# Optimization experiments

Measured on AMD Instinct MI355X. Metric: run time of the kernel, lower is better.

Reference implementation:

```python
import jax, jax.numpy as jnp
import numpy as np

# --- configuration constants (match init_kwargs) ---
N = 256          # num_oscillators
T = 200          # simulation steps
INTERVAL = 5     # readout_update_interval
OFFSET = 1       # spike_update_offset
DELAY = 10
D = DELAY + 1    # delay-buffer length
K_GLOBAL = 1.0   # global_coupling_strength
STEP_SIZE = 0.1
GAMMA_ATTR = 0.5 # gamma_attraction_strength
DECAY = 0.9      # membrane_decay
THRESH = 1.0
REC_SCALE = 0.1
ALPHA_FIX = 0.5  # fixed_alpha_value (fixed during training)
CLS_START = 50   # classifier_start_step
SURR_BETA = 4.0  # surrogate-gradient sharpness
NUM_CLASSES = 10


def _spike(u):
    # Heaviside forward, sigmoid surrogate backward (straight-through)
    sg = jax.nn.sigmoid(SURR_BETA * u)
    hard = (u > 0).astype(u.dtype)
    return sg + jax.lax.stop_gradient(hard - sg)


def _forward(x, theta0, W_init, omega, W_ro, W_gate, W_rec, W_fb, W_cls, b_cls):
    B = x.shape[0]
    P = W_gate.shape[1]  # num_pixels = H*W*C
    xf = x.reshape(B, -1)
    gamma0 = jnp.tanh(xf @ W_init)                 # ReadoutLayer.initialize_gamma_from_input -> [B,N]
    buf0 = jnp.tile(theta0[None], (D, 1, 1))       # theta delay buffer [D,B,N]
    zN = jnp.zeros((B, N), x.dtype)
    zP = jnp.zeros((B, P), x.dtype)
    carry0 = (theta0, gamma0, zN, zP, zP, zN, buf0)  # theta, gamma, gate, membrane, spikes, fb-activity a, buffer

    def step(carry, s):
        theta, gamma, gate, mem, spk, a, buf = carry
        # --- KuramotoLayer: dtheta_i = omega_i + K/N * sum_j (1 + W_ij*alpha) sin(th_j - th_i) + attr*gamma_i
        # top-down connectivity W_ij = a_i a_j is rank-1, so the coupling sum is computed exactly in O(N).
        sin_t = jnp.sin(theta); cos_t = jnp.cos(theta)
        S = sin_t.sum(-1, keepdims=True); C = cos_t.sum(-1, keepdims=True)
        base = cos_t * S - sin_t * C
        as_ = jnp.sum(a * sin_t, -1, keepdims=True)
        ac_ = jnp.sum(a * cos_t, -1, keepdims=True)
        weighted = ALPHA_FIX * (cos_t * a * as_ - sin_t * a * ac_)
        dtheta = omega + (K_GLOBAL / N) * (base + weighted) + GAMMA_ATTR * gamma
        theta = theta + STEP_SIZE * dtheta

        # --- ReadoutLayer.gamma_update + SinusoidalGate every INTERVAL steps
        def ro_upd(args):
            g = jnp.tanh(theta @ W_ro)
            gt = g * 0.5 * (1.0 + jnp.cos(theta - buf[0]))  # gate from delayed phase difference
            return g, gt
        gamma, gate = jax.lax.cond((s % INTERVAL) == 0, ro_upd, lambda args: args, (gamma, gate))

        # --- SNNLayer.forward_step + TopDownFeedback on offset spike-update steps
        def sp_upd(args):
            mem_, spk_, a_ = args
            cur = gate @ W_gate + REC_SCALE * (spk_ @ W_rec)
            mem_ = DECAY * mem_ * (1.0 - spk_) + cur       # leaky membrane with reset
            spk_ = _spike(mem_ - THRESH)
            a_ = jnp.tanh(spk_ @ W_fb)                     # per-oscillator feedback activity
            return mem_, spk_, a_
        m_sp = (((s - OFFSET) % INTERVAL) == 0) & (s > OFFSET)
        mem, spk, a = jax.lax.cond(m_sp, sp_upd, lambda args: args, (mem, spk, a))

        buf = jnp.concatenate([buf[1:], theta[None]], axis=0)
        return (theta, gamma, gate, mem, spk, a, buf), spk

    _, spk_hist = jax.lax.scan(step, carry0, jnp.arange(1, T + 1))
    spike_trace = jnp.transpose(spk_hist, (1, 0, 2))       # [B,T,P]
    rate = jnp.mean(spike_trace[:, CLS_START:, :], axis=1) # SNNLayer.classify: mean firing rate
    logits = rate @ W_cls + b_cls
    return logits


def setup_inputs() -> dict:
    key = jax.random.key(0)
    ks = jax.random.split(key, 10)
    B, H, W, C = 32, 32, 32, 3
    P = H * W * C
    x = jax.random.normal(ks[0], (B, H, W, C), jnp.float32)
    theta0 = jax.random.normal(ks[1], (B, N), jnp.float32)
    W_init = jax.random.normal(ks[2], (P, N), jnp.float32) / np.sqrt(P).astype(np.float32)
    omega = jax.random.normal(ks[3], (N,), jnp.float32) * 0.5
    W_ro = jax.random.normal(ks[4], (N, N), jnp.float32) / np.sqrt(N).astype(np.float32)
    W_gate = jax.random.normal(ks[5], (N, P), jnp.float32) / np.sqrt(N).astype(np.float32)
    W_rec = jax.random.normal(ks[6], (P, P), jnp.float32) / np.sqrt(P).astype(np.float32)
    W_fb = jax.random.normal(ks[7], (P, N), jnp.float32) / np.sqrt(P).astype(np.float32)
    W_cls = jax.random.normal(ks[8], (P, NUM_CLASSES), jnp.float32) / np.sqrt(P).astype(np.float32)
    b_cls = jnp.zeros((NUM_CLASSES,), jnp.float32)
    return dict(x=x, theta0=theta0, W_init=W_init, omega=omega, W_ro=W_ro,
                W_gate=W_gate, W_rec=W_rec, W_fb=W_fb, W_cls=W_cls, b_cls=b_cls)


def reference(x, theta0, W_init, omega, W_ro, W_gate, W_rec, W_fb, W_cls, b_cls):
    return _forward(x, theta0, W_init, omega, W_ro, W_gate, W_rec, W_fb, W_cls, b_cls)
```

## Files before the change

### kernel.cpp

```cpp
#include <hip/hip_runtime.h>
#include <cstdint>
#include <cstddef>

#define BB 32
#define NN 256
#define PP 3072
#define NG 192
#define RING 16

typedef unsigned short u16;

__global__ __launch_bounds__(512) void k_init(
    const float* __restrict__ x, const float* __restrict__ W_init,
    double* __restrict__ gpartI, double* __restrict__ memD,
    double* __restrict__ a_g, float* __restrict__ rate,
    u16* __restrict__ maskA, u16* __restrict__ maskB) {
  const int blk = blockIdx.x, tid = threadIdx.x;
  if (blk < 192) {
    const int b = blk / 6, sub = blk % 6;
    __shared__ double xl[512];
    xl[tid] = (double)x[(size_t)b * PP + sub * 512 + tid];
    __syncthreads();
    const int osc = tid & 255, kh = tid >> 8;
    const float* wp = W_init + (size_t)(sub * 512 + kh * 256) * NN + osc;
    const double* xp = xl + kh * 256;
    double a0 = 0, a1 = 0, a2 = 0, a3 = 0, a4 = 0, a5 = 0, a6 = 0, a7 = 0;
    for (int r = 0; r < 256; r += 8) {
      a0 += xp[r + 0] * (double)wp[(size_t)(r + 0) * NN];
      a1 += xp[r + 1] * (double)wp[(size_t)(r + 1) * NN];
      a2 += xp[r + 2] * (double)wp[(size_t)(r + 2) * NN];
      a3 += xp[r + 3] * (double)wp[(size_t)(r + 3) * NN];
      a4 += xp[r + 4] * (double)wp[(size_t)(r + 4) * NN];
      a5 += xp[r + 5] * (double)wp[(size_t)(r + 5) * NN];
      a6 += xp[r + 6] * (double)wp[(size_t)(r + 6) * NN];
      a7 += xp[r + 7] * (double)wp[(size_t)(r + 7) * NN];
    }
    double acc = ((a0 + a1) + (a2 + a3)) + ((a4 + a5) + (a6 + a7));
    __syncthreads();
    __shared__ double hl[256];
    if (kh) hl[osc] = acc;
    __syncthreads();
    if (!kh) gpartI[((size_t)b * 6 + sub) * 256 + osc] = acc + hl[osc];
  } else {
    const int b = blk - 192;
    for (int i = tid; i < PP; i += 512) {
      memD[(size_t)b * PP + i] = 0.0;
      rate[(size_t)b * PP + i] = 0.f;
    }
    for (int i = tid; i < NG; i += 512) {
      maskA[b * NG + i] = 0;
      maskB[b * NG + i] = 0;
    }
    for (int i = tid; i < NN; i += 512) a_g[b * NN + i] = 0.0;
  }
}

__global__ __launch_bounds__(512, 6) void k_rec(
    const float* __restrict__ W_rec, const u16* __restrict__ listG,
    const int* __restrict__ cntG, const int* __restrict__ cntB,
    double* __restrict__ recPart, const double* __restrict__ gateG,
    const float* __restrict__ W_gate, double* __restrict__ gatePart) {
  __shared__ double gd[16 * 130];
  __shared__ float wt[128 * 16];
  __shared__ double red[256];
  const int g = blockIdx.x, bh = blockIdx.y, z = blockIdx.z, j0 = g * 16;
  const int tid = threadIdx.x;

  if (z < 3) {
    const int qd = tid & 3;
    const int h = (tid >> 2) & 7;
    const int bl = tid >> 5;
    const int b = bh * 16 + bl;
    const int beg = (z == 0) ? 0 : cntB[b * 2 + (z - 1)];
    const int end = (z == 2) ? cntG[b] : cntB[b * 2 + z];
    const u16* lst = listG + (size_t)b * PP;
    const float* wp = W_rec + j0 + 4 * qd;

    double a0 = 0, a1 = 0, a2 = 0, a3 = 0;
    int i = beg + h;
    for (; i + 32 <= end; i += 32) {
      const int r0 = lst[i], r1 = lst[i + 8], r2 = lst[i + 16],
                r3 = lst[i + 24];
      const float4 f0 = *(const float4*)(wp + (size_t)r0 * PP);
      const float4 f1 = *(const float4*)(wp + (size_t)r1 * PP);
      const float4 f2 = *(const float4*)(wp + (size_t)r2 * PP);
      const float4 f3 = *(const float4*)(wp + (size_t)r3 * PP);
      a0 += (double)f0.x; a1 += (double)f0.y;
      a2 += (double)f0.z; a3 += (double)f0.w;
      a0 += (double)f1.x; a1 += (double)f1.y;
      a2 += (double)f1.z; a3 += (double)f1.w;
      a0 += (double)f2.x; a1 += (double)f2.y;
      a2 += (double)f2.z; a3 += (double)f2.w;
      a0 += (double)f3.x; a1 += (double)f3.y;
      a2 += (double)f3.z; a3 += (double)f3.w;
    }
    for (; i < end; i += 8) {
      const float4 f = *(const float4*)(wp + (size_t)lst[i] * PP);
      a0 += (double)f.x; a1 += (double)f.y;
      a2 += (double)f.z; a3 += (double)f.w;
    }
    a0 += __shfl_xor(a0, 4); a0 += __shfl_xor(a0, 8); a0 += __shfl_xor(a0, 16);
    a1 += __shfl_xor(a1, 4); a1 += __shfl_xor(a1, 8); a1 += __shfl_xor(a1, 16);
    a2 += __shfl_xor(a2, 4); a2 += __shfl_xor(a2, 8); a2 += __shfl_xor(a2, 16);
    a3 += __shfl_xor(a3, 4); a3 += __shfl_xor(a3, 8); a3 += __shfl_xor(a3, 16);
    if (h == 0) {
      double* dst = recPart + ((size_t)z * BB + b) * PP + j0 + 4 * qd;
      dst[0] = a0; dst[1] = a1; dst[2] = a2; dst[3] = a3;
    }
  } else {
    const int zh = z - 3;
    for (int i = tid; i < 2048; i += 512) {
      gd[(i >> 7) * 130 + (i & 127)] =
          gateG[(size_t)(bh * 16 + (i >> 7)) * 256 + zh * 128 + (i & 127)];
      wt[i] = W_gate[(size_t)(zh * 128 + (i >> 4)) * PP + j0 + (i & 15)];
    }
    __syncthreads();
    const int pi = tid & 15, bl = (tid >> 4) & 15, hq = tid >> 8;
    const int b = bh * 16 + bl, p = j0 + pi, pid = tid & 255;
    double s0 = 0, s1 = 0, s2 = 0, s3 = 0, s4 = 0, s5 = 0, s6 = 0, s7 = 0;
    const double* gq = gd + bl * 130 + hq * 64;
    const float* wq = wt + hq * 64 * 16 + pi;
    for (int k = 0; k < 64; k += 8) {
      s0 += gq[k + 0] * (double)wq[(k + 0) * 16];
      s1 += gq[k + 1] * (double)wq[(k + 1) * 16];
      s2 += gq[k + 2] * (double)wq[(k + 2) * 16];
      s3 += gq[k + 3] * (double)wq[(k + 3) * 16];
      s4 += gq[k + 4] * (double)wq[(k + 4) * 16];
      s5 += gq[k + 5] * (double)wq[(k + 5) * 16];
      s6 += gq[k + 6] * (double)wq[(k + 6) * 16];
      s7 += gq[k + 7] * (double)wq[(k + 7) * 16];
    }
    double vg = ((s0 + s1) + (s2 + s3)) + ((s4 + s5) + (s6 + s7));
    if (hq) red[pid] = vg;
    __syncthreads();
    if (!hq) gatePart[((size_t)zh * BB + b) * PP + p] = vg + red[pid];
  }
}

__global__ __launch_bounds__(512) void k_fin(
    const u16* __restrict__ mask_rd, u16* __restrict__ mask_wr,
    double* __restrict__ memD, const double* __restrict__ gatePart,
    const double* __restrict__ recPart, float* __restrict__ rate, int accum) {
  const int g = blockIdx.x, tid = threadIdx.x;
  const int pi = tid & 15, b = tid >> 4;
  const int p = g * 16 + pi;
  const size_t idx = (size_t)b * PP + p;
  const double vgs = gatePart[idx] + gatePart[(size_t)BB * PP + idx];
  const double vrs = (recPart[idx] + recPart[(size_t)BB * PP + idx]) +
                     recPart[(size_t)2 * BB * PP + idx];
  const double cur = vgs + 0.1 * vrs;
  const double so = (double)((mask_rd[b * NG + g] >> pi) & 1);
  const double mv = 0.9 * memD[idx] * (1.0 - so) + cur;
  const double sv = (mv - 1.0 > 0.0) ? 1.0 : 0.0;
  memD[idx] = mv;
  if (accum) rate[idx] += (float)sv;
  unsigned long long bal = __ballot(sv > 0.5);
  const int lane = tid & 63;
  if ((lane & 15) == 0)
    mask_wr[b * NG + g] = (u16)((bal >> (16 * (lane >> 4))) & 0xFFFFull);
}

__global__ __launch_bounds__(256) void k_fb(
    const u16* __restrict__ spk_mask, u16* __restrict__ listG,
    int* __restrict__ cntG, int* __restrict__ cntB,
    const float* __restrict__ W_fb, double* __restrict__ a_part) {
  const int b = blockIdx.x, y = blockIdx.y, tid = threadIdx.x;
  __shared__ int pc[NG], sc[NG];
  __shared__ u16 m_l[NG];
  __shared__ u16 list_l[PP];
  if (tid < NG) {
    m_l[tid] = spk_mask[b * NG + tid];
    pc[tid] = __popc((unsigned int)m_l[tid]);
    sc[tid] = pc[tid];
  }
  __syncthreads();
  for (int d = 1; d < NG; d <<= 1) {
    int v = 0;
    if (tid < NG) v = sc[tid] + ((tid >= d) ? sc[tid - d] : 0);
    __syncthreads();
    if (tid < NG) sc[tid] = v;
    __syncthreads();
  }
  const int total = sc[NG - 1];
  if (tid < NG) {
    int off = sc[tid] - pc[tid];
    unsigned int m = m_l[tid];
    while (m) {
      int bit = __builtin_ctz(m);
      m &= m - 1;
      list_l[off++] = (u16)(tid * 16 + bit);
    }
  }
  __syncthreads();
  if (y == 0) {
    for (int i = tid; i < total; i += 256) listG[(size_t)b * PP + i] = list_l[i];
    if (tid == 0) {
      cntG[b] = total;
      cntB[b * 2 + 0] = sc[63];
      cntB[b * 2 + 1] = sc[127];
    }
  }
  const int j = tid;
  double c0 = 0, c1 = 0, c2 = 0, c3 = 0, c4 = 0, c5 = 0, c6 = 0, c7 = 0;
  int i = y;
  for (; i + 128 <= total; i += 128) {
    c0 += (double)W_fb[(size_t)list_l[i + 0] * NN + j];
    c1 += (double)W_fb[(size_t)list_l[i + 16] * NN + j];
    c2 += (double)W_fb[(size_t)list_l[i + 32] * NN + j];
    c3 += (double)W_fb[(size_t)list_l[i + 48] * NN + j];
    c4 += (double)W_fb[(size_t)list_l[i + 64] * NN + j];
    c5 += (double)W_fb[(size_t)list_l[i + 80] * NN + j];
    c6 += (double)W_fb[(size_t)list_l[i + 96] * NN + j];
    c7 += (double)W_fb[(size_t)list_l[i + 112] * NN + j];
  }
  double acc = ((c0 + c1) + (c2 + c3)) + ((c4 + c5) + (c6 + c7));
  for (; i < total; i += 16) acc += (double)W_fb[(size_t)list_l[i] * NN + j];
  a_part[((size_t)b * 16 + y) * NN + j] = acc;
}

__global__ __launch_bounds__(512) void k_theta(
    double* __restrict__ ring, double* __restrict__ gamma_g,
    double* __restrict__ a_g, double* __restrict__ gateG,
    const double* __restrict__ a_part, const float* __restrict__ theta0,
    const float* __restrict__ omega, const float* __restrict__ W_ro,
    const double* __restrict__ gpartI, int* __restrict__ cntG,
    int* __restrict__ cntB, int k2) {
  const int b = blockIdx.x, tid = threadIdx.x;
  const int j = tid & 255, q = tid >> 8;
  const int lane = tid & 63, wid = tid >> 6;
  __shared__ double th[256];
  __shared__ double red[16];
  __shared__ double qpart[256];

  const int s0 = 5 * k2 + 1, s1 = 5 * k2 + 5;
  double new_a = 0.0;
  if (k2 > 0) {
    double s = 0.0;
#pragma unroll
    for (int u = 0; u < 8; ++u)
      s += a_part[((size_t)b * 16 + q * 8 + u) * NN + j];
    if (q) qpart[j] = s;
    __syncthreads();
    if (!q) new_a = tanh(s + qpart[j]);
    __syncthreads();
  }

  double t = 0.0, aj = 0.0, gm = 0.0, om = 0.0;
  if (!q) {
    om = (double)omega[j];
    if (k2 == 0) {
      double s = 0.0;
      for (int c6 = 0; c6 < 6; ++c6) s += gpartI[((size_t)b * 6 + c6) * 256 + j];
      gm = tanh(s);
      t = (double)theta0[b * NN + j];
      ring[0 * BB * NN + b * NN + j] = t;
      if (tid == 0) {
        cntG[b] = 0;
        cntB[b * 2 + 0] = 0;
        cntB[b * 2 + 1] = 0;
      }
    } else {
      t = ring[((s0 - 1) & (RING - 1)) * BB * NN + b * NN + j];
      aj = a_g[b * NN + j];
      gm = gamma_g[b * NN + j];
    }
  }

  for (int s = s0; s <= s1; ++s) {
    if (!q && k2 > 0 && s == s0 + 1) {
      aj = new_a;
      a_g[b * NN + j] = aj;
    }
    double sn = 0.0, cs = 0.0;
    if (!q) sincos(t, &sn, &cs);
    double r0 = sn, r1 = cs, r2 = aj * sn, r3 = aj * cs;
#pragma unroll
    for (int o = 32; o; o >>= 1) {
      r0 += __shfl_down(r0, o);
      r1 += __shfl_down(r1, o);
      r2 += __shfl_down(r2, o);
      r3 += __shfl_down(r3, o);
    }
    if (lane == 0 && wid < 4) {
      red[wid * 4 + 0] = r0;
      red[wid * 4 + 1] = r1;
      red[wid * 4 + 2] = r2;
      red[wid * 4 + 3] = r3;
    }
    __syncthreads();
    double S = red[0] + red[4] + red[8] + red[12];
    double C = red[1] + red[5] + red[9] + red[13];
    double AS = red[2] + red[6] + red[10] + red[14];
    double AC = red[3] + red[7] + red[11] + red[15];
    __syncthreads();
    if (!q) {
      double base = cs * S - sn * C;
      double wgt = 0.5 * (cs * aj * AS - sn * aj * AC);
      t = t + 0.1 * (om + (1.0 / 256.0) * (base + wgt) + 0.5 * gm);
      ring[(s & (RING - 1)) * BB * NN + b * NN + j] = t;
    }
  }
  if (!q) th[j] = t;
  __syncthreads();
  {
    double c0 = 0, c1 = 0, c2 = 0, c3 = 0, c4 = 0, c5 = 0, c6 = 0, c7 = 0;
    const float* wp = W_ro + j;
    const int i0 = q * 128;
    for (int i = 0; i < 128; i += 8) {
      c0 += th[i0 + i + 0] * (double)wp[(size_t)(i0 + i + 0) * NN];
      c1 += th[i0 + i + 1] * (double)wp[(size_t)(i0 + i + 1) * NN];
      c2 += th[i0 + i + 2] * (double)wp[(size_t)(i0 + i + 2) * NN];
      c3 += th[i0 + i + 3] * (double)wp[(size_t)(i0 + i + 3) * NN];
      c4 += th[i0 + i + 4] * (double)wp[(size_t)(i0 + i + 4) * NN];
      c5 += th[i0 + i + 5] * (double)wp[(size_t)(i0 + i + 5) * NN];
      c6 += th[i0 + i + 6] * (double)wp[(size_t)(i0 + i + 6) * NN];
      c7 += th[i0 + i + 7] * (double)wp[(size_t)(i0 + i + 7) * NN];
    }
    double acc = ((c0 + c1) + (c2 + c3)) + ((c4 + c5) + (c6 + c7));
    if (q) qpart[j] = acc;
    __syncthreads();
    if (!q) {
      double gnew = tanh(acc + qpart[j]);
      gamma_g[b * NN + j] = gnew;
      int sd = s1 - 11;
      if (sd < 0) sd = 0;
      double dly = ring[(sd & (RING - 1)) * BB * NN + b * NN + j];
      double gt = gnew * 0.5 * (1.0 + cos(t - dly));
      gateG[(size_t)b * 256 + j] = gt;
    }
  }
}

__global__ __launch_bounds__(256) void k_cls(const float* __restrict__ rate,
                                             const float* __restrict__ Wcls,
                                             const float* __restrict__ bcls,
                                             float* __restrict__ out) {
  const int b = blockIdx.x, t = threadIdx.x;
  double acc[10];
#pragma unroll
  for (int c = 0; c < 10; ++c) acc[c] = 0.0;
  for (int p = t; p < PP; p += 256) {
    double r = (double)rate[(size_t)b * PP + p] / 30.0;
#pragma unroll
    for (int c = 0; c < 10; ++c) acc[c] += r * (double)Wcls[(size_t)p * 10 + c];
  }
  __shared__ double sh[10][256];
#pragma unroll
  for (int c = 0; c < 10; ++c) sh[c][t] = acc[c];
  __syncthreads();
  for (int off = 128; off; off >>= 1) {
    if (t < off)
#pragma unroll
      for (int c = 0; c < 10; ++c) sh[c][t] += sh[c][t + off];
    __syncthreads();
  }
  if (t < 10) out[b * 10 + t] = (float)(sh[t][0] + (double)bcls[t]);
}

extern "C" void kernel_launch(void* const* d_in, const int* in_sizes, int n_in,
                              void* d_out, int out_size, void* d_ws,
                              size_t ws_size, hipStream_t stream) {
  const float* x = (const float*)d_in[0];
  const float* theta0 = (const float*)d_in[1];
  const float* W_init = (const float*)d_in[2];
  const float* omega = (const float*)d_in[3];
  const float* W_ro = (const float*)d_in[4];
  const float* W_gate = (const float*)d_in[5];
  const float* W_rec = (const float*)d_in[6];
  const float* W_fb = (const float*)d_in[7];
  const float* W_cls = (const float*)d_in[8];
  const float* b_cls = (const float*)d_in[9];

  char* w = (char*)d_ws;
  size_t off = 0;
  auto alloc = [&](size_t sz) -> void* {
    void* p = w + off;
    off = (off + sz + 255) & ~(size_t)255;
    return p;
  };
  double* ring = (double*)alloc((size_t)RING * BB * NN * 8);
  double* gamma = (double*)alloc((size_t)BB * NN * 8);
  double* a_g = (double*)alloc((size_t)BB * NN * 8);
  double* gateG = (double*)alloc((size_t)BB * NN * 8);
  double* memD = (double*)alloc((size_t)BB * PP * 8);
  float* rate = (float*)alloc((size_t)BB * PP * 4);
  u16* maskA = (u16*)alloc((size_t)BB * NG * 2);
  u16* maskB = (u16*)alloc((size_t)BB * NG * 2);
  u16* listG = (u16*)alloc((size_t)BB * PP * 2);
  int* cntG = (int*)alloc((size_t)BB * 4);
  int* cntB = (int*)alloc((size_t)BB * 2 * 4);
  double* gpartI = (double*)alloc((size_t)BB * 6 * 256 * 8);
  double* a_part = (double*)alloc((size_t)BB * 16 * NN * 8);
  double* recPart = (double*)alloc((size_t)3 * BB * PP * 8);
  double* gatePart = (double*)alloc((size_t)2 * BB * PP * 8);

  k_init<<<224, 512, 0, stream>>>(x, W_init, gpartI, memD, a_g, rate, maskA,
                                  maskB);
  k_theta<<<32, 512, 0, stream>>>(ring, gamma, a_g, gateG, a_part, theta0,
                                  omega, W_ro, gpartI, cntG, cntB, 0);
  for (int k = 1; k < 40; ++k) {
    const u16* mrd = (k & 1) ? maskA : maskB;
    u16* mwr = (k & 1) ? maskB : maskA;
    k_rec<<<dim3(192, 2, 5), 512, 0, stream>>>(W_rec, listG, cntG, cntB,
                                               recPart, gateG, W_gate,
                                               gatePart);
    k_fin<<<192, 512, 0, stream>>>(mrd, mwr, memD, gatePart, recPart, rate,
                                   (k >= 10) ? 1 : 0);
    k_fb<<<dim3(32, 16), 256, 0, stream>>>(mwr, listG, cntG, cntB, W_fb,
                                           a_part);
    k_theta<<<32, 512, 0, stream>>>(ring, gamma, a_g, gateG, a_part, theta0,
                                    omega, W_ro, gpartI, cntG, cntB, k);
  }
  k_cls<<<32, 256, 0, stream>>>(rate, W_cls, b_cls, (float*)d_out);
}
```

Before: 2.115 ms.

## Merge theta update with recurrent gather and fold gate matvec into fin kernel

The recurrent-weight gather (previously in k_rec) now runs as extra blocks inside the theta-update kernel, since both depend only on the spike list from the previous k_fb. The gate-current matvec moves into k_fin, which loads all 32 gate rows and a 256x16 W_gate slice into shared memory, so the gatePart buffer and its round-trip are gone. This cuts one launch per iteration and lets the tiny 32-block theta kernel overlap with the gather blocks. In exchange, k_fin now redoes a 256-long dot per output with a large shared-memory footprint, which may lower occupancy. Counter initialisation moves to k_init.

```diff
diff --git a/kernel.cpp b/kernel.cpp
--- a/kernel.cpp
+++ b/kernel.cpp
@@ -14,7 +14,8 @@
     const float* __restrict__ x, const float* __restrict__ W_init,
     double* __restrict__ gpartI, double* __restrict__ memD,
     double* __restrict__ a_g, float* __restrict__ rate,
-    u16* __restrict__ maskA, u16* __restrict__ maskB) {
+    u16* __restrict__ maskA, u16* __restrict__ maskB, int* __restrict__ cntG,
+    int* __restrict__ cntB) {
   const int blk = blockIdx.x, tid = threadIdx.x;
   if (blk < 192) {
     const int b = blk / 6, sub = blk % 6;
@@ -52,21 +53,31 @@
       maskB[b * NG + i] = 0;
     }
     for (int i = tid; i < NN; i += 512) a_g[b * NN + i] = 0.0;
-  }
-}
-
-__global__ __launch_bounds__(512, 6) void k_rec(
-    const float* __restrict__ W_rec, const u16* __restrict__ listG,
-    const int* __restrict__ cntG, const int* __restrict__ cntB,
-    double* __restrict__ recPart, const double* __restrict__ gateG,
-    const float* __restrict__ W_gate, double* __restrict__ gatePart) {
-  __shared__ double gd[16 * 130];
-  __shared__ float wt[128 * 16];
-  __shared__ double red[256];
-  const int g = blockIdx.x, bh = blockIdx.y, z = blockIdx.z, j0 = g * 16;
-  const int tid = threadIdx.x;
-
-  if (z < 3) {
+    if (tid == 0) {
+      cntG[b] = 0;
+      cntB[b * 2 + 0] = 0;
+      cntB[b * 2 + 1] = 0;
+    }
+  }
+}
+
+__global__ __launch_bounds__(512) void k_tg(
+    double* __restrict__ ring, double* __restrict__ gamma_g,
+    double* __restrict__ a_g, double* __restrict__ gateG,
+    const double* __restrict__ a_part, const float* __restrict__ theta0,
+    const float* __restrict__ omega, const float* __restrict__ W_ro,
+    const double* __restrict__ gpartI, const float* __restrict__ W_rec,
+    const u16* __restrict__ listG, const int* __restrict__ cntG,
+    const int* __restrict__ cntB, double* __restrict__ recPart, int k2) {
+  const int blk = blockIdx.x, tid = threadIdx.x;
+  __shared__ double th[256];
+  __shared__ double red[16];
+  __shared__ double qpart[256];
+
+  if (blk >= 32) {
+    if (k2 >= 39) return;
+    const int w = blk - 32;
+    const int g = w % 192, bh = (w / 192) & 1, z = w / 384, j0 = g * 16;
     const int qd = tid & 3;
     const int h = (tid >> 2) & 7;
     const int bl = tid >> 5;
@@ -85,19 +96,14 @@
       const float4 f1 = *(const float4*)(wp + (size_t)r1 * PP);
       const float4 f2 = *(const float4*)(wp + (size_t)r2 * PP);
       const float4 f3 = *(const float4*)(wp + (size_t)r3 * PP);
-      a0 += (double)f0.x; a1 += (double)f0.y;
-      a2 += (double)f0.z; a3 += (double)f0.w;
-      a0 += (double)f1.x; a1 += (double)f1.y;
-      a2 += (double)f1.z; a3 += (double)f1.w;
-      a0 += (double)f2.x; a1 += (double)f2.y;
-      a2 += (double)f2.z; a3 += (double)f2.w;
-      a0 += (double)f3.x; a1 += (double)f3.y;
-      a2 += (double)f3.z; a3 += (double)f3.w;
+      a0 += (double)f0.x; a1 += (double)f0.y; a2 += (double)f0.z; a3 += (double)f0.w;
+      a0 += (double)f1.x; a1 += (double)f1.y; a2 += (double)f1.z; a3 += (double)f1.w;
+      a0 += (double)f2.x; a1 += (double)f2.y; a2 += (double)f2.z; a3 += (double)f2.w;
+      a0 += (double)f3.x; a1 += (double)f3.y; a2 += (double)f3.z; a3 += (double)f3.w;
     }
     for (; i < end; i += 8) {
       const float4 f = *(const float4*)(wp + (size_t)lst[i] * PP);
-      a0 += (double)f.x; a1 += (double)f.y;
-      a2 += (double)f.z; a3 += (double)f.w;
+      a0 += (double)f.x; a1 += (double)f.y; a2 += (double)f.z; a3 += (double)f.w;
     }
     a0 += __shfl_xor(a0, 4); a0 += __shfl_xor(a0, 8); a0 += __shfl_xor(a0, 16);
     a1 += __shfl_xor(a1, 4); a1 += __shfl_xor(a1, 8); a1 += __shfl_xor(a1, 16);
@@ -107,131 +113,12 @@
       double* dst = recPart + ((size_t)z * BB + b) * PP + j0 + 4 * qd;
       dst[0] = a0; dst[1] = a1; dst[2] = a2; dst[3] = a3;
     }
-  } else {
-    const int zh = z - 3;
-    for (int i = tid; i < 2048; i += 512) {
-      gd[(i >> 7) * 130 + (i & 127)] =
-          gateG[(size_t)(bh * 16 + (i >> 7)) * 256 + zh * 128 + (i & 127)];
-      wt[i] = W_gate[(size_t)(zh * 128 + (i >> 4)) * PP + j0 + (i & 15)];
-    }
-    __syncthreads();
-    const int pi = tid & 15, bl = (tid >> 4) & 15, hq = tid >> 8;
-    const int b = bh * 16 + bl, p = j0 + pi, pid = tid & 255;
-    double s0 = 0, s1 = 0, s2 = 0, s3 = 0, s4 = 0, s5 = 0, s6 = 0, s7 = 0;
-    const double* gq = gd + bl * 130 + hq * 64;
-    const float* wq = wt + hq * 64 * 16 + pi;
-    for (int k = 0; k < 64; k += 8) {
-      s0 += gq[k + 0] * (double)wq[(k + 0) * 16];
-      s1 += gq[k + 1] * (double)wq[(k + 1) * 16];
-      s2 += gq[k + 2] * (double)wq[(k + 2) * 16];
-      s3 += gq[k + 3] * (double)wq[(k + 3) * 16];
-      s4 += gq[k + 4] * (double)wq[(k + 4) * 16];
-      s5 += gq[k + 5] * (double)wq[(k + 5) * 16];
-      s6 += gq[k + 6] * (double)wq[(k + 6) * 16];
-      s7 += gq[k + 7] * (double)wq[(k + 7) * 16];
-    }
-    double vg = ((s0 + s1) + (s2 + s3)) + ((s4 + s5) + (s6 + s7));
-    if (hq) red[pid] = vg;
-    __syncthreads();
-    if (!hq) gatePart[((size_t)zh * BB + b) * PP + p] = vg + red[pid];
-  }
-}
-
-__global__ __launch_bounds__(512) void k_fin(
-    const u16* __restrict__ mask_rd, u16* __restrict__ mask_wr,
-    double* __restrict__ memD, const double* __restrict__ gatePart,
-    const double* __restrict__ recPart, float* __restrict__ rate, int accum) {
-  const int g = blockIdx.x, tid = threadIdx.x;
-  const int pi = tid & 15, b = tid >> 4;
-  const int p = g * 16 + pi;
-  const size_t idx = (size_t)b * PP + p;
-  const double vgs = gatePart[idx] + gatePart[(size_t)BB * PP + idx];
-  const double vrs = (recPart[idx] + recPart[(size_t)BB * PP + idx]) +
-                     recPart[(size_t)2 * BB * PP + idx];
-  const double cur = vgs + 0.1 * vrs;
-  const double so = (double)((mask_rd[b * NG + g] >> pi) & 1);
-  const double mv = 0.9 * memD[idx] * (1.0 - so) + cur;
-  const double sv = (mv - 1.0 > 0.0) ? 1.0 : 0.0;
-  memD[idx] = mv;
-  if (accum) rate[idx] += (float)sv;
-  unsigned long long bal = __ballot(sv > 0.5);
-  const int lane = tid & 63;
-  if ((lane & 15) == 0)
-    mask_wr[b * NG + g] = (u16)((bal >> (16 * (lane >> 4))) & 0xFFFFull);
-}
-
-__global__ __launch_bounds__(256) void k_fb(
-    const u16* __restrict__ spk_mask, u16* __restrict__ listG,
-    int* __restrict__ cntG, int* __restrict__ cntB,
-    const float* __restrict__ W_fb, double* __restrict__ a_part) {
-  const int b = blockIdx.x, y = blockIdx.y, tid = threadIdx.x;
-  __shared__ int pc[NG], sc[NG];
-  __shared__ u16 m_l[NG];
-  __shared__ u16 list_l[PP];
-  if (tid < NG) {
-    m_l[tid] = spk_mask[b * NG + tid];
-    pc[tid] = __popc((unsigned int)m_l[tid]);
-    sc[tid] = pc[tid];
-  }
-  __syncthreads();
-  for (int d = 1; d < NG; d <<= 1) {
-    int v = 0;
-    if (tid < NG) v = sc[tid] + ((tid >= d) ? sc[tid - d] : 0);
-    __syncthreads();
-    if (tid < NG) sc[tid] = v;
-    __syncthreads();
-  }
-  const int total = sc[NG - 1];
-  if (tid < NG) {
-    int off = sc[tid] - pc[tid];
-    unsigned int m = m_l[tid];
-    while (m) {
-      int bit = __builtin_ctz(m);
-      m &= m - 1;
-      list_l[off++] = (u16)(tid * 16 + bit);
-    }
-  }
-  __syncthreads();
-  if (y == 0) {
-    for (int i = tid; i < total; i += 256) listG[(size_t)b * PP + i] = list_l[i];
-    if (tid == 0) {
-      cntG[b] = total;
-      cntB[b * 2 + 0] = sc[63];
-      cntB[b * 2 + 1] = sc[127];
-    }
-  }
-  const int j = tid;
-  double c0 = 0, c1 = 0, c2 = 0, c3 = 0, c4 = 0, c5 = 0, c6 = 0, c7 = 0;
-  int i = y;
-  for (; i + 128 <= total; i += 128) {
-    c0 += (double)W_fb[(size_t)list_l[i + 0] * NN + j];
-    c1 += (double)W_fb[(size_t)list_l[i + 16] * NN + j];
-    c2 += (double)W_fb[(size_t)list_l[i + 32] * NN + j];
-    c3 += (double)W_fb[(size_t)list_l[i + 48] * NN + j];
-    c4 += (double)W_fb[(size_t)list_l[i + 64] * NN + j];
-    c5 += (double)W_fb[(size_t)list_l[i + 80] * NN + j];
-    c6 += (double)W_fb[(size_t)list_l[i + 96] * NN + j];
-    c7 += (double)W_fb[(size_t)list_l[i + 112] * NN + j];
-  }
-  double acc = ((c0 + c1) + (c2 + c3)) + ((c4 + c5) + (c6 + c7));
-  for (; i < total; i += 16) acc += (double)W_fb[(size_t)list_l[i] * NN + j];
-  a_part[((size_t)b * 16 + y) * NN + j] = acc;
-}
-
-__global__ __launch_bounds__(512) void k_theta(
-    double* __restrict__ ring, double* __restrict__ gamma_g,
-    double* __restrict__ a_g, double* __restrict__ gateG,
-    const double* __restrict__ a_part, const float* __restrict__ theta0,
-    const float* __restrict__ omega, const float* __restrict__ W_ro,
-    const double* __restrict__ gpartI, int* __restrict__ cntG,
-    int* __restrict__ cntB, int k2) {
-  const int b = blockIdx.x, tid = threadIdx.x;
+    return;
+  }
+
+  const int b = blk;
   const int j = tid & 255, q = tid >> 8;
   const int lane = tid & 63, wid = tid >> 6;
-  __shared__ double th[256];
-  __shared__ double red[16];
-  __shared__ double qpart[256];
-
   const int s0 = 5 * k2 + 1, s1 = 5 * k2 + 5;
   double new_a = 0.0;
   if (k2 > 0) {
@@ -254,11 +141,6 @@
       gm = tanh(s);
       t = (double)theta0[b * NN + j];
       ring[0 * BB * NN + b * NN + j] = t;
-      if (tid == 0) {
-        cntG[b] = 0;
-        cntB[b * 2 + 0] = 0;
-        cntB[b * 2 + 1] = 0;
-      }
     } else {
       t = ring[((s0 - 1) & (RING - 1)) * BB * NN + b * NN + j];
       aj = a_g[b * NN + j];
@@ -329,6 +211,121 @@
       gateG[(size_t)b * 256 + j] = gt;
     }
   }
+}
+
+__global__ __launch_bounds__(512) void k_fin(
+    const u16* __restrict__ mask_rd, u16* __restrict__ mask_wr,
+    double* __restrict__ memD, const double* __restrict__ gateG,
+    const float* __restrict__ W_gate, const double* __restrict__ recPart,
+    float* __restrict__ rate, int accum) {
+  __shared__ double gd[32 * 258];
+  __shared__ float wt[256 * 16];
+  const int g = blockIdx.x, tid = threadIdx.x, j0 = g * 16;
+  for (int i = tid; i < 8192; i += 512)
+    gd[(i >> 8) * 258 + (i & 255)] = gateG[(size_t)(i >> 8) * 256 + (i & 255)];
+  for (int i = tid; i < 4096; i += 512)
+    wt[i] = W_gate[(size_t)(i >> 4) * PP + j0 + (i & 15)];
+  __syncthreads();
+
+  const int pi = tid & 15, b = tid >> 4;
+  const double* gq = gd + b * 258;
+  const float* wq = wt + pi;
+  double ch0, ch1, ch2, ch3;
+  {
+    double c[4];
+#pragma unroll
+    for (int cq = 0; cq < 4; ++cq) {
+      const double* gc = gq + cq * 64;
+      const float* wc = wq + cq * 64 * 16;
+      double s0 = 0, s1 = 0, s2 = 0, s3 = 0, s4 = 0, s5 = 0, s6 = 0, s7 = 0;
+      for (int k = 0; k < 64; k += 8) {
+        s0 += gc[k + 0] * (double)wc[(k + 0) * 16];
+        s1 += gc[k + 1] * (double)wc[(k + 1) * 16];
+        s2 += gc[k + 2] * (double)wc[(k + 2) * 16];
+        s3 += gc[k + 3] * (double)wc[(k + 3) * 16];
+        s4 += gc[k + 4] * (double)wc[(k + 4) * 16];
+        s5 += gc[k + 5] * (double)wc[(k + 5) * 16];
+        s6 += gc[k + 6] * (double)wc[(k + 6) * 16];
+        s7 += gc[k + 7] * (double)wc[(k + 7) * 16];
+      }
+      c[cq] = ((s0 + s1) + (s2 + s3)) + ((s4 + s5) + (s6 + s7));
+    }
+    ch0 = c[0]; ch1 = c[1]; ch2 = c[2]; ch3 = c[3];
+  }
+  const double vgs = (ch0 + ch1) + (ch2 + ch3);
+
+  const int p = j0 + pi;
+  const size_t idx = (size_t)b * PP + p;
+  const double vrs = (recPart[idx] + recPart[(size_t)BB * PP + idx]) +
+                     recPart[(size_t)2 * BB * PP + idx];
+  const double cur = vgs + 0.1 * vrs;
+  const double so = (double)((mask_rd[b * NG + g] >> pi) & 1);
+  const double mv = 0.9 * memD[idx] * (1.0 - so) + cur;
+  const double sv = (mv - 1.0 > 0.0) ? 1.0 : 0.0;
+  memD[idx] = mv;
+  if (accum) rate[idx] += (float)sv;
+  unsigned long long bal = __ballot(sv > 0.5);
+  const int lane = tid & 63;
+  if ((lane & 15) == 0)
+    mask_wr[b * NG + g] = (u16)((bal >> (16 * (lane >> 4))) & 0xFFFFull);
+}
+
+__global__ __launch_bounds__(256) void k_fb(
+    const u16* __restrict__ spk_mask, u16* __restrict__ listG,
+    int* __restrict__ cntG, int* __restrict__ cntB,
+    const float* __restrict__ W_fb, double* __restrict__ a_part) {
+  const int b = blockIdx.x, y = blockIdx.y, tid = threadIdx.x;
+  __shared__ int pc[NG], sc[NG];
+  __shared__ u16 m_l[NG];
+  __shared__ u16 list_l[PP];
+  if (tid < NG) {
+    m_l[tid] = spk_mask[b * NG + tid];
+    pc[tid] = __popc((unsigned int)m_l[tid]);
+    sc[tid] = pc[tid];
+  }
+  __syncthreads();
+  for (int d = 1; d < NG; d <<= 1) {
+    int v = 0;
+    if (tid < NG) v = sc[tid] + ((tid >= d) ? sc[tid - d] : 0);
+    __syncthreads();
+    if (tid < NG) sc[tid] = v;
+    __syncthreads();
+  }
+  const int total = sc[NG - 1];
+  if (tid < NG) {
+    int off = sc[tid] - pc[tid];
+    unsigned int m = m_l[tid];
+    while (m) {
+      int bit = __builtin_ctz(m);
+      m &= m - 1;
+      list_l[off++] = (u16)(tid * 16 + bit);
+    }
+  }
+  __syncthreads();
+  if (y == 0) {
+    for (int i = tid; i < total; i += 256) listG[(size_t)b * PP + i] = list_l[i];
+    if (tid == 0) {
+      cntG[b] = total;
+      cntB[b * 2 + 0] = sc[63];
+      cntB[b * 2 + 1] = sc[127];
+    }
+  }
+  const int j = tid;
+  double c0 = 0, c1 = 0, c2 = 0, c3 = 0, c4 = 0, c5 = 0, c6 = 0, c7 = 0;
+  int i = y;
+  for (; i + 128 <= total; i += 128) {
+    c0 += (double)W_fb[(size_t)list_l[i + 0] * NN + j];
+    c1 += (double)W_fb[(size_t)list_l[i + 16] * NN + j];
+    c2 += (double)W_fb[(size_t)list_l[i + 32] * NN + j];
+    c3 += (double)W_fb[(size_t)list_l[i + 48] * NN + j];
+    c4 += (double)W_fb[(size_t)list_l[i + 64] * NN + j];
+    c5 += (double)W_fb[(size_t)list_l[i + 80] * NN + j];
+    c6 += (double)W_fb[(size_t)list_l[i + 96] * NN + j];
+    c7 += (double)W_fb[(size_t)list_l[i + 112] * NN + j];
+  }
+  double acc = ((c0 + c1) + (c2 + c3)) + ((c4 + c5) + (c6 + c7));
+  for (; i < total; i += 16) acc += (double)W_fb[(size_t)list_l[i] * NN + j];
+  a_part[((size_t)b * 16 + y) * NN + j] = acc;
 }
 
 __global__ __launch_bounds__(256) void k_cls(const float* __restrict__ rate,
@@ -392,24 +389,22 @@
   double* gpartI = (double*)alloc((size_t)BB * 6 * 256 * 8);
   double* a_part = (double*)alloc((size_t)BB * 16 * NN * 8);
   double* recPart = (double*)alloc((size_t)3 * BB * PP * 8);
-  double* gatePart = (double*)alloc((size_t)2 * BB * PP * 8);
 
   k_init<<<224, 512, 0, stream>>>(x, W_init, gpartI, memD, a_g, rate, maskA,
-                                  maskB);
-  k_theta<<<32, 512, 0, stream>>>(ring, gamma, a_g, gateG, a_part, theta0,
-                                  omega, W_ro, gpartI, cntG, cntB, 0);
+                                  maskB, cntG, cntB);
+  k_tg<<<1184, 512, 0, stream>>>(ring, gamma, a_g, gateG, a_part, theta0,
+                                 omega, W_ro, gpartI, W_rec, listG, cntG, cntB,
+                                 recPart, 0);
   for (int k = 1; k < 40; ++k) {
     const u16* mrd = (k & 1) ? maskA : maskB;
     u16* mwr = (k & 1) ? maskB : maskA;
-    k_rec<<<dim3(192, 2, 5), 512, 0, stream>>>(W_rec, listG, cntG, cntB,
-                                               recPart, gateG, W_gate,
-                                               gatePart);
-    k_fin<<<192, 512, 0, stream>>>(mrd, mwr, memD, gatePart, recPart, rate,
-                                   (k >= 10) ? 1 : 0);
+    k_fin<<<192, 512, 0, stream>>>(mrd, mwr, memD, gateG, W_gate, recPart,
+                                   rate, (k >= 10) ? 1 : 0);
     k_fb<<<dim3(32, 16), 256, 0, stream>>>(mwr, listG, cntG, cntB, W_fb,
                                            a_part);
-    k_theta<<<32, 512, 0, stream>>>(ring, gamma, a_g, gateG, a_part, theta0,
-                                    omega, W_ro, gpartI, cntG, cntB, k);
+    k_tg<<<1184, 512, 0, stream>>>(ring, gamma, a_g, gateG, a_part, theta0,
+                                   omega, W_ro, gpartI, W_rec, listG, cntG,
+                                   cntB, recPart, k);
   }
   k_cls<<<32, 256, 0, stream>>>(rate, W_cls, b_cls, (float*)d_out);
 }
```

Result: faster. 1.974 ms (-6.7%).
